# Kernel optimization log

Hardware: AMD Instinct MI355X
Metric: run time of the kernel (lower is better)

## Reference

```python
import jax, jax.numpy as jnp
import numpy as np
from jax import lax

B, S, D, H = 2, 2048, 1024, 16
DH = D // H
KERNELS = (3, 5)
NK = len(KERNELS)
COUT = D // NK  # channels per conv branch


def setup_inputs() -> dict:
    key = jax.random.key(0)
    ks = jax.random.split(key, 12)
    w = lambda k, shp: (jax.random.normal(k, shp, dtype=jnp.float32) * 0.02)
    inp = {
        "q": jax.random.normal(ks[0], (B, S, D), dtype=jnp.float32),
        "k": jax.random.normal(ks[1], (B, S, D), dtype=jnp.float32),
        "v": jax.random.normal(ks[2], (B, S, D), dtype=jnp.float32),
        "mask": jnp.ones((B, S, S), dtype=jnp.int32),
        "Wq": w(ks[3], (D, D)),
        "Wk": w(ks[4], (D, D)),
        "Wv": w(ks[5], (D, D)),
        "Wo": w(ks[6], (D, D)),
        "bo": jnp.zeros((D,), dtype=jnp.float32),
        "conv_w0": w(ks[7], (COUT, D, KERNELS[0])),  # OIH
        "conv_b0": jnp.zeros((COUT,), dtype=jnp.float32),
        "conv_w1": w(ks[8], (COUT, D, KERNELS[1])),
        "conv_b1": jnp.zeros((COUT,), dtype=jnp.float32),
        "gate": jnp.ones((H,), dtype=jnp.float32),
    }
    return inp


def _split_heads(x):  # [B,S,D] -> [B,H,S,DH]
    return x.reshape(B, S, H, DH).transpose(0, 2, 1, 3)


def _conv1d_same(x_ncl, w_oik, b, ksz):
    pad = ksz // 2
    y = lax.conv_general_dilated(
        x_ncl, w_oik, window_strides=(1,), padding=[(pad, pad)],
        dimension_numbers=("NCH", "OIH", "NCH"))
    return y + b[None, :, None]


def reference(q, k, v, mask, Wq, Wk, Wv, Wo, bo,
              conv_w0, conv_b0, conv_w1, conv_b1, gate):
    qh = _split_heads(q @ Wq.T)
    kh = _split_heads(k @ Wk.T)
    vh = _split_heads(v @ Wv.T)

    # conv-derived K: operate on raw k in NCL layout, concat channel-wise
    k_ncl = k.transpose(0, 2, 1)  # [B,D,S]
    c0 = _conv1d_same(k_ncl, conv_w0, conv_b0, KERNELS[0])
    c1 = _conv1d_same(k_ncl, conv_w1, conv_b1, KERNELS[1])
    k_conv = jnp.concatenate([c0, c1], axis=1).transpose(0, 2, 1)  # [B,S,D]
    kch = _split_heads(k_conv)

    g = jax.nn.sigmoid(gate).reshape(1, H, 1, 1)
    scale = 1.0 / np.sqrt(DH).astype(np.float32)
    attn = ((1.0 - g) * jnp.einsum("bhqd,bhkd->bhqk", qh, kh)
            + g * jnp.einsum("bhqd,bhkd->bhqk", qh, kch)) * scale
    attn = jnp.where(mask[:, None, :, :] == 0, jnp.float32(-1e9), attn)
    attn = jax.nn.softmax(attn, axis=-1)

    out = jnp.einsum("bhqk,bhkd->bhqd", attn, vh)  # [B,H,S,DH]
    out = out.transpose(0, 2, 1, 3).reshape(B, S, D)
    return out @ Wo.T + bo
```

## Files before the change

### kernel.cpp

```cpp
#include <hip/hip_runtime.h>
#include <math.h>

#define Bb 2
#define Ss 2048
#define Dd 1024
#define Hh 16
#define SP 2052

typedef unsigned short u16;
typedef __bf16 bf16x8 __attribute__((ext_vector_type(8)));
typedef float f32x4 __attribute__((ext_vector_type(4)));
typedef unsigned short u16x8 __attribute__((ext_vector_type(8)));

__device__ __forceinline__ u16 f2bf(float f) {
    union { float f; unsigned int u; } c; c.f = f;
    unsigned int u = c.u + 0x7FFFu + ((c.u >> 16) & 1u);
    return (u16)(u >> 16);
}

__device__ __forceinline__ void gload16(const void* g, void* l) {
    __builtin_amdgcn_global_load_lds(
        (const __attribute__((address_space(1))) void*)g,
        (__attribute__((address_space(3))) void*)l, 16, 0, 0);
}

__global__ void prep_weights(const float* __restrict__ Wq, const float* __restrict__ Wk,
                             const float* __restrict__ Wv, const float* __restrict__ Wo,
                             const float* __restrict__ w0, const float* __restrict__ b0,
                             const float* __restrict__ w1, const float* __restrict__ b1,
                             const float* __restrict__ gate,
                             u16* __restrict__ wqs, u16* __restrict__ wvb, u16* __restrict__ wob,
                             u16* __restrict__ Wc0, u16* __restrict__ Wc1, float* __restrict__ bc)
{
    int idx = blockIdx.x * 256 + threadIdx.x;
    const int NW = 1024 * 1024;
    if (idx < NW) { wqs[idx] = f2bf(Wq[idx] * 0.18033688011112042f); return; }
    idx -= NW;
    if (idx < NW) { wvb[idx] = f2bf(Wv[idx]); return; }
    idx -= NW;
    if (idx < NW) { wob[idx] = f2bf(Wo[idx]); return; }
    idx -= NW;
    if (idx < 512 * 3072) {
        int c = idx / 3072, rem = idx % 3072, t = rem >> 10, d = rem & 1023;
        float g = 1.f / (1.f + expf(-gate[c >> 6]));
        float v = g * w0[(c * 1024 + d) * 3 + t];
        if (t == 1) v += (1.f - g) * Wk[c * 1024 + d];
        Wc0[idx] = f2bf(v);
        return;
    }
    idx -= 512 * 3072;
    if (idx < 512 * 5120) {
        int c = idx / 5120, rem = idx % 5120, t = rem >> 10, d = rem & 1023;
        int cg = c + 512;
        float g = 1.f / (1.f + expf(-gate[cg >> 6]));
        float v = g * w1[(c * 1024 + d) * 5 + t];
        if (t == 2) v += (1.f - g) * Wk[cg * 1024 + d];
        Wc1[idx] = f2bf(v);
        return;
    }
    idx -= 512 * 5120;
    if (idx < 1024) {
        float g = 1.f / (1.f + expf(-gate[idx >> 6]));
        bc[idx] = g * (idx < 512 ? b0[idx] : b1[idx - 512]);
    }
}

__global__ void convert_inputs(const float* __restrict__ q, const float* __restrict__ k,
                               const float* __restrict__ v,
                               u16* __restrict__ qbf, u16* __restrict__ kbf, u16* __restrict__ vbf)
{
    int idx = blockIdx.x * 256 + threadIdx.x;
    const int per = (Bb * SP * Dd) / 8;
    int which = idx / per;
    if (which >= 3) return;
    int e = (idx - which * per) * 8;
    const float* src = which == 0 ? q : which == 1 ? k : v;
    u16* dst = which == 0 ? qbf : which == 1 ? kbf : vbf;
    int rp = e >> 10, col = e & 1023;
    int b = rp / SP, r = rp - b * SP;
    u16x8 o;
    if (r >= 2 && r < SP - 2) {
        const float* s = &src[((size_t)b * Ss + (r - 2)) * Dd + col];
        float4 lo = *(const float4*)s, hi = *(const float4*)(s + 4);
        o[0] = f2bf(lo.x); o[1] = f2bf(lo.y); o[2] = f2bf(lo.z); o[3] = f2bf(lo.w);
        o[4] = f2bf(hi.x); o[5] = f2bf(hi.y); o[6] = f2bf(hi.z); o[7] = f2bf(hi.w);
    } else {
        #pragma unroll
        for (int j = 0; j < 8; j++) o[j] = 0;
    }
    *(u16x8*)&dst[e] = o;
}

__global__ void mask_prep(const int* __restrict__ mask, unsigned int* __restrict__ bits,
                          int* __restrict__ rowflags)
{
    int row = blockIdx.x;
    int lane = threadIdx.x;
    const int* mp = mask + (size_t)row * Ss + lane * 32;
    unsigned int w = 0;
    #pragma unroll
    for (int j = 0; j < 32; j += 4) {
        int4 m4 = *(const int4*)&mp[j];
        if (m4.x != 0) w |= 1u << j;
        if (m4.y != 0) w |= 1u << (j + 1);
        if (m4.z != 0) w |= 1u << (j + 2);
        if (m4.w != 0) w |= 1u << (j + 3);
    }
    bits[(size_t)row * 64 + lane] = w;
    int anyz = __any(w != 0xFFFFFFFFu);
    if (lane == 0) rowflags[row] = anyz;
}

__global__ __launch_bounds__(256) void gemm_multi(
    const u16* __restrict__ qbf, const u16* __restrict__ kbf, const u16* __restrict__ vbf,
    const u16* __restrict__ wqs, const u16* __restrict__ wvb,
    const u16* __restrict__ Wc0, const u16* __restrict__ Wc1,
    u16* __restrict__ Qp, u16* __restrict__ Vp, u16* __restrict__ Keff,
    const float* __restrict__ bc)
{
    __shared__ u16 As[128 * 32];
    __shared__ u16 Bs[128 * 32];
    int tid = threadIdx.x, lane = tid & 63, wave = tid >> 6;
    int waveM = (wave >> 1) * 64, waveN = (wave & 1) * 64;

    int bid = blockIdx.x;
    const u16 *A, *B;
    u16* C;
    const float* bias = nullptr;
    int K, rowOff, colOff, mBase, nBase;
    if (bid < 256) {
        A = qbf; B = wqs; C = Qp; K = 1024; rowOff = 2; colOff = 0;
        nBase = (bid & 7) * 128; mBase = (bid >> 3) * 128;
    } else if (bid < 512) {
        bid -= 256;
        A = vbf; B = wvb; C = Vp; K = 1024; rowOff = 2; colOff = 0;
        nBase = (bid & 7) * 128; mBase = (bid >> 3) * 128;
    } else if (bid < 640) {
        bid -= 512;
        A = kbf; B = Wc0; C = Keff; K = 3072; rowOff = 1; colOff = 0; bias = bc;
        nBase = (bid & 3) * 128; mBase = (bid >> 2) * 128;
    } else {
        bid -= 640;
        A = kbf; B = Wc1; C = Keff; K = 5120; rowOff = 0; colOff = 512; bias = bc;
        nBase = (bid & 3) * 128; mBase = (bid >> 2) * 128;
    }

    f32x4 acc[4][4];
    #pragma unroll
    for (int i = 0; i < 4; i++)
        #pragma unroll
        for (int j = 0; j < 4; j++) acc[i][j] = (f32x4){0.f, 0.f, 0.f, 0.f};

    for (int k0 = 0; k0 < K; k0 += 32) {
        __syncthreads();
        #pragma unroll
        for (int cc = 0; cc < 2; cc++) {
            int rbase = (wave * 2 + cc) * 16;
            int r = rbase + (lane >> 2);
            int gm = mBase + r;
            int grow = (gm >> 11) * SP + (gm & 2047) + rowOff + (k0 >> 10);
            int csrc = (lane & 3) ^ (r & 3);
            gload16(A + (size_t)grow * 1024 + (k0 & 1023) + csrc * 8, &As[rbase * 32]);
            int gn = nBase + r;
            gload16(B + (size_t)gn * K + k0 + csrc * 8, &Bs[rbase * 32]);
        }
        __syncthreads();

        bf16x8 af[4], bfr[4];
        #pragma unroll
        for (int t = 0; t < 4; t++) {
            int mrow = waveM + t * 16 + (lane & 15);
            af[t] = *(const bf16x8*)&As[mrow * 32 + (((lane >> 4) ^ (mrow & 3))) * 8];
            int nrow = waveN + t * 16 + (lane & 15);
            bfr[t] = *(const bf16x8*)&Bs[nrow * 32 + (((lane >> 4) ^ (nrow & 3))) * 8];
        }
        #pragma unroll
        for (int mt = 0; mt < 4; mt++)
            #pragma unroll
            for (int nt = 0; nt < 4; nt++)
                acc[mt][nt] = __builtin_amdgcn_mfma_f32_16x16x32_bf16(
                    af[mt], bfr[nt], acc[mt][nt], 0, 0, 0);
    }

    #pragma unroll
    for (int mt = 0; mt < 4; mt++)
        #pragma unroll
        for (int nt = 0; nt < 4; nt++)
            #pragma unroll
            for (int r = 0; r < 4; r++) {
                int row = mBase + waveM + mt * 16 + (lane >> 4) * 4 + r;
                int gcol = nBase + waveN + nt * 16 + (lane & 15);
                float v = acc[mt][nt][r];
                if (bias) v += bias[colOff + gcol];
                C[(size_t)row * 1024 + colOff + gcol] = f2bf(v);
            }
}

__global__ __launch_bounds__(256) void gemm_out(
    const u16* __restrict__ A, const u16* __restrict__ Bw,
    float* __restrict__ Cf32, const float* __restrict__ bias)
{
    __shared__ u16 As[128 * 32];
    __shared__ u16 Bs[128 * 32];
    int tid = threadIdx.x, lane = tid & 63, wave = tid >> 6;
    int waveM = (wave >> 1) * 64, waveN = (wave & 1) * 64;
    int mBase = blockIdx.y * 128, nBase = blockIdx.x * 128;
    const int K = 1024;

    f32x4 acc[4][4];
    #pragma unroll
    for (int i = 0; i < 4; i++)
        #pragma unroll
        for (int j = 0; j < 4; j++) acc[i][j] = (f32x4){0.f, 0.f, 0.f, 0.f};

    for (int k0 = 0; k0 < K; k0 += 32) {
        __syncthreads();
        #pragma unroll
        for (int cc = 0; cc < 2; cc++) {
            int rbase = (wave * 2 + cc) * 16;
            int r = rbase + (lane >> 2);
            int gm = mBase + r;
            int grow = (gm >> 11) * SP + (gm & 2047) + 2;
            int csrc = (lane & 3) ^ (r & 3);
            gload16(A + (size_t)grow * 1024 + k0 + csrc * 8, &As[rbase * 32]);
            int gn = nBase + r;
            gload16(Bw + (size_t)gn * K + k0 + csrc * 8, &Bs[rbase * 32]);
        }
        __syncthreads();

        bf16x8 af[4], bfr[4];
        #pragma unroll
        for (int t = 0; t < 4; t++) {
            int mrow = waveM + t * 16 + (lane & 15);
            af[t] = *(const bf16x8*)&As[mrow * 32 + (((lane >> 4) ^ (mrow & 3))) * 8];
            int nrow = waveN + t * 16 + (lane & 15);
            bfr[t] = *(const bf16x8*)&Bs[nrow * 32 + (((lane >> 4) ^ (nrow & 3))) * 8];
        }
        #pragma unroll
        for (int mt = 0; mt < 4; mt++)
            #pragma unroll
            for (int nt = 0; nt < 4; nt++)
                acc[mt][nt] = __builtin_amdgcn_mfma_f32_16x16x32_bf16(
                    af[mt], bfr[nt], acc[mt][nt], 0, 0, 0);
    }

    #pragma unroll
    for (int mt = 0; mt < 4; mt++)
        #pragma unroll
        for (int nt = 0; nt < 4; nt++)
            #pragma unroll
            for (int r = 0; r < 4; r++) {
                int row = mBase + waveM + mt * 16 + (lane >> 4) * 4 + r;
                int gcol = nBase + waveN + nt * 16 + (lane & 15);
                Cf32[(size_t)row * 1024 + gcol] = acc[mt][nt][r] + bias[gcol];
            }
}

__global__ __launch_bounds__(256) void vtrans_kernel(const u16* __restrict__ Vp,
                                                     u16* __restrict__ Vt)
{
    __shared__ u16 t[64 * 64];
    int bid = blockIdx.x;
    int st = bid & 31, h = (bid >> 5) & 15, b = bid >> 9;
    int s0 = st * 64;
    int tid = threadIdx.x;
    #pragma unroll
    for (int w = 0; w < 2; w++) {
        int f = tid + w * 256;
        int row = f >> 3, c = f & 7;
        int p = c ^ (row & 7);
        u16x8 v = *(const u16x8*)&Vp[(size_t)(b * Ss + s0 + row) * Dd + h * 64 + c * 8];
        *(u16x8*)&t[row * 64 + p * 8] = v;
    }
    __syncthreads();
    #pragma unroll
    for (int w = 0; w < 2; w++) {
        int f = tid + w * 256;
        int d = f >> 3, s8 = (f & 7) * 8;
        u16x8 v;
        #pragma unroll
        for (int j = 0; j < 8; j++) {
            int s = s8 + j;
            v[j] = t[s * 64 + (((d >> 3) ^ (s & 7))) * 8 + (d & 7)];
        }
        *(u16x8*)&Vt[((size_t)(b * Hh + h) * 64 + d) * Ss + s0 + s8] = v;
    }
}

__global__ __launch_bounds__(256) void flash_kernel(
    const u16* __restrict__ Qp, const u16* __restrict__ Keff, const u16* __restrict__ Vt,
    const unsigned int* __restrict__ maskbits, const int* __restrict__ rowflags,
    u16* __restrict__ AO)
{
    __shared__ u16 Qs[128 * 64];
    __shared__ u16 Ks[64 * 64];
    __shared__ u16 Ps[4][32 * 64];
    int tid = threadIdx.x, lane = tid & 63, wave = tid >> 6;
    int q0 = blockIdx.x * 128, h = blockIdx.y, b = blockIdx.z;

    #pragma unroll
    for (int cc = 0; cc < 4; cc++) {
        int rbase = (wave * 4 + cc) * 8;
        int r = rbase + (lane >> 3);
        int csrc = (lane & 7) ^ (r & 7);
        gload16(Qp + (size_t)(b * Ss + q0 + r) * Dd + h * 64 + csrc * 8, &Qs[rbase * 64]);
    }

    int anyz = 0;
    #pragma unroll
    for (int mt = 0; mt < 2; mt++)
        #pragma unroll
        for (int r = 0; r < 4; r++)
            anyz |= rowflags[b * Ss + q0 + wave * 32 + mt * 16 + (lane >> 4) * 4 + r];
    bool doMask = __any(anyz);

    float lrow[2][4];
    f32x4 oa[2][4];
    #pragma unroll
    for (int mt = 0; mt < 2; mt++) {
        #pragma unroll
        for (int r = 0; r < 4; r++) lrow[mt][r] = 0.f;
        #pragma unroll
        for (int nt = 0; nt < 4; nt++) oa[mt][nt] = (f32x4){0.f, 0.f, 0.f, 0.f};
    }

    __syncthreads();

    bf16x8 qa[2][2];
    #pragma unroll
    for (int mt = 0; mt < 2; mt++)
        #pragma unroll
        for (int ks = 0; ks < 2; ks++) {
            int mr = wave * 32 + mt * 16 + (lane & 15);
            int c = ks * 4 + (lane >> 4);
            qa[mt][ks] = *(const bf16x8*)&Qs[mr * 64 + (c ^ (mr & 7)) * 8];
        }

    const u16* vbase = Vt + (size_t)(b * Hh + h) * 64 * Ss;

    for (int k0 = 0; k0 < Ss; k0 += 64) {
        #pragma unroll
        for (int cc = 0; cc < 2; cc++) {
            int rbase = (wave * 2 + cc) * 8;
            int r = rbase + (lane >> 3);
            int csrc = (lane & 7) ^ (r & 7);
            gload16(Keff + (size_t)(b * Ss + k0 + r) * Dd + h * 64 + csrc * 8, &Ks[rbase * 64]);
        }
        __syncthreads();

        f32x4 sa[2][4];
        #pragma unroll
        for (int mt = 0; mt < 2; mt++)
            #pragma unroll
            for (int nt = 0; nt < 4; nt++) sa[mt][nt] = (f32x4){0.f, 0.f, 0.f, 0.f};
        bf16x8 kb[4][2];
        #pragma unroll
        for (int nt = 0; nt < 4; nt++)
            #pragma unroll
            for (int ks = 0; ks < 2; ks++) {
                int nr = nt * 16 + (lane & 15);
                int c = ks * 4 + (lane >> 4);
                kb[nt][ks] = *(const bf16x8*)&Ks[nr * 64 + (c ^ (nr & 7)) * 8];
            }
        #pragma unroll
        for (int mt = 0; mt < 2; mt++)
            #pragma unroll
            for (int nt = 0; nt < 4; nt++)
                #pragma unroll
                for (int ks = 0; ks < 2; ks++)
                    sa[mt][nt] = __builtin_amdgcn_mfma_f32_16x16x32_bf16(
                        qa[mt][ks], kb[nt][ks], sa[mt][nt], 0, 0, 0);

        bf16x8 vf[4][2];
        #pragma unroll
        for (int nt = 0; nt < 4; nt++)
            #pragma unroll
            for (int ks = 0; ks < 2; ks++) {
                int d = nt * 16 + (lane & 15);
                int kc = k0 + ks * 32 + (lane >> 4) * 8;
                vf[nt][ks] = *(const bf16x8*)&vbase[(size_t)d * Ss + kc];
            }

        if (doMask) {
            #pragma unroll
            for (int mt = 0; mt < 2; mt++)
                #pragma unroll
                for (int r = 0; r < 4; r++) {
                    int qrow = q0 + wave * 32 + mt * 16 + (lane >> 4) * 4 + r;
                    const unsigned int* mb = &maskbits[((size_t)b * Ss + qrow) * 64 + (k0 >> 5)];
                    unsigned int w0m = mb[0], w1m = mb[1];
                    #pragma unroll
                    for (int nt = 0; nt < 4; nt++) {
                        int col = nt * 16 + (lane & 15);
                        unsigned int w = (col & 32) ? w1m : w0m;
                        if (!((w >> (col & 31)) & 1u)) sa[mt][nt][r] = -1.442695e9f;
                    }
                }
        }

        #pragma unroll
        for (int mt = 0; mt < 2; mt++)
            #pragma unroll
            for (int r = 0; r < 4; r++) {
                float p0 = __builtin_amdgcn_exp2f(sa[mt][0][r]);
                float p1 = __builtin_amdgcn_exp2f(sa[mt][1][r]);
                float p2 = __builtin_amdgcn_exp2f(sa[mt][2][r]);
                float p3 = __builtin_amdgcn_exp2f(sa[mt][3][r]);
                sa[mt][0][r] = p0; sa[mt][1][r] = p1;
                sa[mt][2][r] = p2; sa[mt][3][r] = p3;
                lrow[mt][r] += (p0 + p1) + (p2 + p3);
            }

        u16* pw = Ps[wave];
        #pragma unroll
        for (int mt = 0; mt < 2; mt++)
            #pragma unroll
            for (int nt = 0; nt < 4; nt++)
                #pragma unroll
                for (int r = 0; r < 4; r++) {
                    int row = mt * 16 + (lane >> 4) * 4 + r;
                    int col = nt * 16 + (lane & 15);
                    pw[row * 64 + (((col >> 3) ^ (row & 7))) * 8 + (col & 7)] =
                        f2bf(sa[mt][nt][r]);
                }

        bf16x8 pa[2][2];
        #pragma unroll
        for (int mt = 0; mt < 2; mt++)
            #pragma unroll
            for (int ks = 0; ks < 2; ks++) {
                int row = mt * 16 + (lane & 15);
                int c = ks * 4 + (lane >> 4);
                pa[mt][ks] = *(const bf16x8*)&pw[row * 64 + (c ^ (row & 7)) * 8];
            }
        #pragma unroll
        for (int mt = 0; mt < 2; mt++)
            #pragma unroll
            for (int nt = 0; nt < 4; nt++)
                #pragma unroll
                for (int ks = 0; ks < 2; ks++)
                    oa[mt][nt] = __builtin_amdgcn_mfma_f32_16x16x32_bf16(
                        pa[mt][ks], vf[nt][ks], oa[mt][nt], 0, 0, 0);

        __syncthreads();
    }

    #pragma unroll
    for (int mt = 0; mt < 2; mt++)
        #pragma unroll
        for (int r = 0; r < 4; r++) {
            float rs = lrow[mt][r];
            #pragma unroll
            for (int d = 1; d < 16; d <<= 1) rs += __shfl_xor(rs, d, 64);
            float inv = 1.f / rs;
            int qrow = q0 + wave * 32 + mt * 16 + (lane >> 4) * 4 + r;
            size_t rowbase = ((size_t)b * SP + 2 + qrow) * Dd + h * 64;
            #pragma unroll
            for (int nt = 0; nt < 4; nt++)
                AO[rowbase + nt * 16 + (lane & 15)] = f2bf(oa[mt][nt][r] * inv);
        }
}

extern "C" void kernel_launch(void* const* d_in, const int* in_sizes, int n_in,
                              void* d_out, int out_size, void* d_ws, size_t ws_size,
                              hipStream_t stream)
{
    (void)in_sizes; (void)n_in; (void)out_size; (void)ws_size;
    const float* q    = (const float*)d_in[0];
    const float* k    = (const float*)d_in[1];
    const float* v    = (const float*)d_in[2];
    const int*   mask = (const int*)d_in[3];
    const float* Wq   = (const float*)d_in[4];
    const float* Wk   = (const float*)d_in[5];
    const float* Wv   = (const float*)d_in[6];
    const float* Wo   = (const float*)d_in[7];
    const float* bo   = (const float*)d_in[8];
    const float* w0   = (const float*)d_in[9];
    const float* b0   = (const float*)d_in[10];
    const float* w1   = (const float*)d_in[11];
    const float* b1   = (const float*)d_in[12];
    const float* gate = (const float*)d_in[13];
    float* out = (float*)d_out;

    char* p = (char*)d_ws;
    const size_t nPad = (size_t)Bb * SP * Dd;
    const size_t nBSD = (size_t)Bb * Ss * Dd;
    u16* qbf  = (u16*)p;            p += nPad * 2;
    u16* kbf  = (u16*)p;            p += nPad * 2;
    u16* vbf  = (u16*)p;            p += nPad * 2;
    u16* Qp   = (u16*)p;            p += nBSD * 2;
    u16* Keff = (u16*)p;            p += nBSD * 2;
    u16* Vp   = (u16*)p;            p += nBSD * 2;
    u16* Vt   = (u16*)p;            p += nBSD * 2;
    u16* wqs  = (u16*)p;            p += (size_t)Dd * Dd * 2;
    u16* wvb  = (u16*)p;            p += (size_t)Dd * Dd * 2;
    u16* wob  = (u16*)p;            p += (size_t)Dd * Dd * 2;
    u16* Wc0  = (u16*)p;            p += (size_t)512 * 3072 * 2;
    u16* Wc1  = (u16*)p;            p += (size_t)512 * 5120 * 2;
    float* bc = (float*)p;          p += 1024 * 4;
    unsigned int* mbits = (unsigned int*)p; p += (size_t)Bb * Ss * 64 * 4;
    int* rflags = (int*)p;          p += (size_t)Bb * Ss * 4;
    u16* AO = vbf;

    {
        int total = 3 * 1024 * 1024 + 512 * 3072 + 512 * 5120 + 1024;
        hipLaunchKernelGGL(prep_weights, dim3((total + 255) / 256), dim3(256), 0, stream,
                           Wq, Wk, Wv, Wo, w0, b0, w1, b1, gate,
                           wqs, wvb, wob, Wc0, Wc1, bc);
    }
    {
        int total = 3 * (Bb * SP * Dd) / 8;
        hipLaunchKernelGGL(convert_inputs, dim3((total + 255) / 256), dim3(256), 0, stream,
                           q, k, v, qbf, kbf, vbf);
    }
    hipLaunchKernelGGL(mask_prep, dim3(Bb * Ss), dim3(64), 0, stream, mask, mbits, rflags);

    hipLaunchKernelGGL(gemm_multi, dim3(768), dim3(256), 0, stream,
                       qbf, kbf, vbf, wqs, wvb, Wc0, Wc1, Qp, Vp, Keff, bc);
    hipLaunchKernelGGL(vtrans_kernel, dim3(Bb * Hh * (Ss / 64)), dim3(256), 0, stream, Vp, Vt);
    hipLaunchKernelGGL(flash_kernel, dim3(Ss / 128, Hh, Bb), dim3(256), 0, stream,
                       Qp, Keff, Vt, mbits, rflags, AO);
    hipLaunchKernelGGL(gemm_out, dim3(8, 32), dim3(256), 0, stream,
                       AO, wob, out, bo);
}
```

Baseline: 412.2 us.

## Split-K the conv GEMMs and rebalance per-block work in gemm_multi

The conv-derived K projections (K=3072 and K=5120) are split along K into 1024/2048-length chunks that write bf16 partial sums. These chunks, plus pairs of Q/V projection tiles, are spread across 768 blocks so every block does about 2048 of K work instead of some blocks doing 5120. A new conv_reduce kernel adds the partials and the bias into Keff. The aim is to remove the load-imbalance tail where the long conv blocks dominate. In exchange it adds an extra launch, partial-sum traffic, and bf16 rounding of the partials, which reduces accuracy.

```diff
diff --git a/kernel.cpp b/kernel.cpp
--- a/kernel.cpp
+++ b/kernel.cpp
@@ -16,6 +16,11 @@
     union { float f; unsigned int u; } c; c.f = f;
     unsigned int u = c.u + 0x7FFFu + ((c.u >> 16) & 1u);
     return (u16)(u >> 16);
+}
+
+__device__ __forceinline__ float bf2f(u16 h) {
+    union { unsigned int u; float f; } c; c.u = ((unsigned int)h) << 16;
+    return c.f;
 }
 
 __device__ __forceinline__ void gload16(const void* g, void* l) {
@@ -111,89 +116,144 @@
     if (lane == 0) rowflags[row] = anyz;
 }
 
+__device__ __forceinline__ void run_gemm_job(
+    const u16* __restrict__ A, const u16* __restrict__ B, u16* __restrict__ C,
+    int strB, int kS, int kL, int mB, int nB, int rO, int Cst,
+    u16* As, u16* Bsh, int lane, int wave, int waveM, int waveN)
+{
+    f32x4 acc[4][4];
+    #pragma unroll
+    for (int i = 0; i < 4; i++)
+        #pragma unroll
+        for (int j = 0; j < 4; j++) acc[i][j] = (f32x4){0.f, 0.f, 0.f, 0.f};
+
+    for (int k0 = kS; k0 < kS + kL; k0 += 32) {
+        __syncthreads();
+        #pragma unroll
+        for (int cc = 0; cc < 2; cc++) {
+            int rbase = (wave * 2 + cc) * 16;
+            int r = rbase + (lane >> 2);
+            int gm = mB + r;
+            int grow = (gm >> 11) * SP + (gm & 2047) + rO + (k0 >> 10);
+            int csrc = (lane & 3) ^ (r & 3);
+            gload16(A + (size_t)grow * 1024 + (k0 & 1023) + csrc * 8, &As[rbase * 32]);
+            int gn = nB + r;
+            gload16(B + (size_t)gn * strB + k0 + csrc * 8, &Bsh[rbase * 32]);
+        }
+        __syncthreads();
+
+        bf16x8 af[4], bfr[4];
+        #pragma unroll
+        for (int t = 0; t < 4; t++) {
+            int mrow = waveM + t * 16 + (lane & 15);
+            af[t] = *(const bf16x8*)&As[mrow * 32 + (((lane >> 4) ^ (mrow & 3))) * 8];
+            int nrow = waveN + t * 16 + (lane & 15);
+            bfr[t] = *(const bf16x8*)&Bsh[nrow * 32 + (((lane >> 4) ^ (nrow & 3))) * 8];
+        }
+        #pragma unroll
+        for (int mt = 0; mt < 4; mt++)
+            #pragma unroll
+            for (int nt = 0; nt < 4; nt++)
+                acc[mt][nt] = __builtin_amdgcn_mfma_f32_16x16x32_bf16(
+                    af[mt], bfr[nt], acc[mt][nt], 0, 0, 0);
+    }
+
+    #pragma unroll
+    for (int mt = 0; mt < 4; mt++)
+        #pragma unroll
+        for (int nt = 0; nt < 4; nt++)
+            #pragma unroll
+            for (int r = 0; r < 4; r++) {
+                int row = mB + waveM + mt * 16 + (lane >> 4) * 4 + r;
+                int gcol = nB + waveN + nt * 16 + (lane & 15);
+                C[(size_t)row * Cst + gcol] = f2bf(acc[mt][nt][r]);
+            }
+}
+
 __global__ __launch_bounds__(256) void gemm_multi(
     const u16* __restrict__ qbf, const u16* __restrict__ kbf, const u16* __restrict__ vbf,
     const u16* __restrict__ wqs, const u16* __restrict__ wvb,
     const u16* __restrict__ Wc0, const u16* __restrict__ Wc1,
-    u16* __restrict__ Qp, u16* __restrict__ Vp, u16* __restrict__ Keff,
-    const float* __restrict__ bc)
+    u16* __restrict__ Qp, u16* __restrict__ Vp,
+    u16* __restrict__ P0a, u16* __restrict__ P0b,
+    u16* __restrict__ P1a, u16* __restrict__ P1b, u16* __restrict__ P1c)
 {
     __shared__ u16 As[128 * 32];
-    __shared__ u16 Bs[128 * 32];
+    __shared__ u16 Bsh[128 * 32];
     int tid = threadIdx.x, lane = tid & 63, wave = tid >> 6;
     int waveM = (wave >> 1) * 64, waveN = (wave & 1) * 64;
 
     int bid = blockIdx.x;
-    const u16 *A, *B;
-    u16* C;
-    const float* bias = nullptr;
-    int K, rowOff, colOff, mBase, nBase;
-    if (bid < 256) {
-        A = qbf; B = wqs; C = Qp; K = 1024; rowOff = 2; colOff = 0;
-        nBase = (bid & 7) * 128; mBase = (bid >> 3) * 128;
+    const u16 *A0, *B0; u16 *C0; int sB0, kS0, kL0, mB0, nB0, rO0, Cs0;
+    const u16 *A1 = nullptr, *B1 = nullptr; u16 *C1 = nullptr;
+    int sB1 = 0, kS1 = 0, kL1 = 0, mB1 = 0, nB1 = 0, rO1 = 0, Cs1 = 0;
+    int njobs = 1;
+
+    if (bid < 128) {
+        int t = bid;
+        A0 = kbf; B0 = Wc0; C0 = P0a; sB0 = 3072; kS0 = 0; kL0 = 2048;
+        mB0 = (t >> 2) * 128; nB0 = (t & 3) * 128; rO0 = 1; Cs0 = 512;
+    } else if (bid < 256) {
+        int t = bid - 128;
+        A0 = kbf; B0 = Wc1; C0 = P1a; sB0 = 5120; kS0 = 0; kL0 = 2048;
+        mB0 = (t >> 2) * 128; nB0 = (t & 3) * 128; rO0 = 0; Cs0 = 512;
+    } else if (bid < 384) {
+        int t = bid - 256;
+        A0 = kbf; B0 = Wc1; C0 = P1b; sB0 = 5120; kS0 = 2048; kL0 = 2048;
+        mB0 = (t >> 2) * 128; nB0 = (t & 3) * 128; rO0 = 0; Cs0 = 512;
     } else if (bid < 512) {
-        bid -= 256;
-        A = vbf; B = wvb; C = Vp; K = 1024; rowOff = 2; colOff = 0;
-        nBase = (bid & 7) * 128; mBase = (bid >> 3) * 128;
-    } else if (bid < 640) {
-        bid -= 512;
-        A = kbf; B = Wc0; C = Keff; K = 3072; rowOff = 1; colOff = 0; bias = bc;
-        nBase = (bid & 3) * 128; mBase = (bid >> 2) * 128;
+        int t = bid - 384;
+        A0 = kbf; B0 = Wc0; C0 = P0b; sB0 = 3072; kS0 = 2048; kL0 = 1024;
+        mB0 = (t >> 2) * 128; nB0 = (t & 3) * 128; rO0 = 1; Cs0 = 512;
+        A1 = kbf; B1 = Wc1; C1 = P1c; sB1 = 5120; kS1 = 4096; kL1 = 1024;
+        mB1 = mB0; nB1 = nB0; rO1 = 0; Cs1 = 512;
+        njobs = 2;
     } else {
-        bid -= 640;
-        A = kbf; B = Wc1; C = Keff; K = 5120; rowOff = 0; colOff = 512; bias = bc;
-        nBase = (bid & 3) * 128; mBase = (bid >> 2) * 128;
-    }
-
-    f32x4 acc[4][4];
-    #pragma unroll
-    for (int i = 0; i < 4; i++)
-        #pragma unroll
-        for (int j = 0; j < 4; j++) acc[i][j] = (f32x4){0.f, 0.f, 0.f, 0.f};
-
-    for (int k0 = 0; k0 < K; k0 += 32) {
-        __syncthreads();
-        #pragma unroll
-        for (int cc = 0; cc < 2; cc++) {
-            int rbase = (wave * 2 + cc) * 16;
-            int r = rbase + (lane >> 2);
-            int gm = mBase + r;
-            int grow = (gm >> 11) * SP + (gm & 2047) + rowOff + (k0 >> 10);
-            int csrc = (lane & 3) ^ (r & 3);
-            gload16(A + (size_t)grow * 1024 + (k0 & 1023) + csrc * 8, &As[rbase * 32]);
-            int gn = nBase + r;
-            gload16(B + (size_t)gn * K + k0 + csrc * 8, &Bs[rbase * 32]);
-        }
-        __syncthreads();
-
-        bf16x8 af[4], bfr[4];
-        #pragma unroll
-        for (int t = 0; t < 4; t++) {
-            int mrow = waveM + t * 16 + (lane & 15);
-            af[t] = *(const bf16x8*)&As[mrow * 32 + (((lane >> 4) ^ (mrow & 3))) * 8];
-            int nrow = waveN + t * 16 + (lane & 15);
-            bfr[t] = *(const bf16x8*)&Bs[nrow * 32 + (((lane >> 4) ^ (nrow & 3))) * 8];
-        }
-        #pragma unroll
-        for (int mt = 0; mt < 4; mt++)
-            #pragma unroll
-            for (int nt = 0; nt < 4; nt++)
-                acc[mt][nt] = __builtin_amdgcn_mfma_f32_16x16x32_bf16(
-                    af[mt], bfr[nt], acc[mt][nt], 0, 0, 0);
-    }
-
-    #pragma unroll
-    for (int mt = 0; mt < 4; mt++)
-        #pragma unroll
-        for (int nt = 0; nt < 4; nt++)
-            #pragma unroll
-            for (int r = 0; r < 4; r++) {
-                int row = mBase + waveM + mt * 16 + (lane >> 4) * 4 + r;
-                int gcol = nBase + waveN + nt * 16 + (lane & 15);
-                float v = acc[mt][nt][r];
-                if (bias) v += bias[colOff + gcol];
-                C[(size_t)row * 1024 + colOff + gcol] = f2bf(v);
-            }
+        int i0 = (bid - 512) * 2, i1 = i0 + 1;
+        if (i0 < 256) { A0 = qbf; B0 = wqs; C0 = Qp; }
+        else { i0 -= 256; A0 = vbf; B0 = wvb; C0 = Vp; }
+        sB0 = 1024; kS0 = 0; kL0 = 1024;
+        mB0 = (i0 >> 3) * 128; nB0 = (i0 & 7) * 128; rO0 = 2; Cs0 = 1024;
+        if (i1 < 256) { A1 = qbf; B1 = wqs; C1 = Qp; }
+        else { i1 -= 256; A1 = vbf; B1 = wvb; C1 = Vp; }
+        sB1 = 1024; kS1 = 0; kL1 = 1024;
+        mB1 = (i1 >> 3) * 128; nB1 = (i1 & 7) * 128; rO1 = 2; Cs1 = 1024;
+        njobs = 2;
+    }
+
+    run_gemm_job(A0, B0, C0, sB0, kS0, kL0, mB0, nB0, rO0, Cs0,
+                 As, Bsh, lane, wave, waveM, waveN);
+    if (njobs == 2)
+        run_gemm_job(A1, B1, C1, sB1, kS1, kL1, mB1, nB1, rO1, Cs1,
+                     As, Bsh, lane, wave, waveM, waveN);
+}
+
+__global__ __launch_bounds__(256) void conv_reduce(
+    const u16* __restrict__ P0a, const u16* __restrict__ P0b,
+    const u16* __restrict__ P1a, const u16* __restrict__ P1b, const u16* __restrict__ P1c,
+    const float* __restrict__ bc, u16* __restrict__ Keff)
+{
+    int idx = blockIdx.x * 256 + threadIdx.x;
+    int e = idx * 8;
+    int r = e >> 9, c = e & 511;
+    u16x8 a0 = *(const u16x8*)&P0a[e];
+    u16x8 b0 = *(const u16x8*)&P0b[e];
+    u16x8 a1 = *(const u16x8*)&P1a[e];
+    u16x8 b1 = *(const u16x8*)&P1b[e];
+    u16x8 c1 = *(const u16x8*)&P1c[e];
+    float bias0[8], bias1[8];
+    *(float4*)&bias0[0] = *(const float4*)&bc[c];
+    *(float4*)&bias0[4] = *(const float4*)&bc[c + 4];
+    *(float4*)&bias1[0] = *(const float4*)&bc[512 + c];
+    *(float4*)&bias1[4] = *(const float4*)&bc[512 + c + 4];
+    u16x8 o0, o1;
+    #pragma unroll
+    for (int j = 0; j < 8; j++) {
+        o0[j] = f2bf(bf2f(a0[j]) + bf2f(b0[j]) + bias0[j]);
+        o1[j] = f2bf(bf2f(a1[j]) + bf2f(b1[j]) + bf2f(c1[j]) + bias1[j]);
+    }
+    *(u16x8*)&Keff[(size_t)r * 1024 + c] = o0;
+    *(u16x8*)&Keff[(size_t)r * 1024 + 512 + c] = o1;
 }
 
 __global__ __launch_bounds__(256) void gemm_out(
@@ -485,6 +545,7 @@
     char* p = (char*)d_ws;
     const size_t nPad = (size_t)Bb * SP * Dd;
     const size_t nBSD = (size_t)Bb * Ss * Dd;
+    const size_t nHalf = (size_t)4096 * 512;
     u16* qbf  = (u16*)p;            p += nPad * 2;
     u16* kbf  = (u16*)p;            p += nPad * 2;
     u16* vbf  = (u16*)p;            p += nPad * 2;
@@ -500,6 +561,11 @@
     float* bc = (float*)p;          p += 1024 * 4;
     unsigned int* mbits = (unsigned int*)p; p += (size_t)Bb * Ss * 64 * 4;
     int* rflags = (int*)p;          p += (size_t)Bb * Ss * 4;
+    u16* P1a = (u16*)p;             p += nHalf * 2;
+    u16* P1b = (u16*)p;             p += nHalf * 2;
+    u16* P1c = (u16*)p;             p += nHalf * 2;
+    u16* P0a = Vt;
+    u16* P0b = Vt + nHalf;
     u16* AO = vbf;
 
     {
@@ -516,7 +582,10 @@
     hipLaunchKernelGGL(mask_prep, dim3(Bb * Ss), dim3(64), 0, stream, mask, mbits, rflags);
 
     hipLaunchKernelGGL(gemm_multi, dim3(768), dim3(256), 0, stream,
-                       qbf, kbf, vbf, wqs, wvb, Wc0, Wc1, Qp, Vp, Keff, bc);
+                       qbf, kbf, vbf, wqs, wvb, Wc0, Wc1, Qp, Vp,
+                       P0a, P0b, P1a, P1b, P1c);
+    hipLaunchKernelGGL(conv_reduce, dim3(1024), dim3(256), 0, stream,
+                       P0a, P0b, P1a, P1b, P1c, bc, Keff);
     hipLaunchKernelGGL(vtrans_kernel, dim3(Bb * Hh * (Ss / 64)), dim3(256), 0, stream, Vp, Vt);
     hipLaunchKernelGGL(flash_kernel, dim3(Ss / 128, Hh, Bb), dim3(256), 0, stream,
                        Qp, Keff, Vt, mbits, rflags, AO);
```

Result: faster. 365.8 us (-11.2%).
